# Kernel tuning notes

Hardware: AMD Instinct MI355X
Metric: run time of the kernel (lower is better)

## Reference

```python
import jax, jax.numpy as jnp
import numpy as np

GROUP_SIZE = 32


def setup_inputs() -> dict:
    key = jax.random.key(0)
    k1, k2 = jax.random.split(key)
    R, L = 4096, 16384
    G = L // GROUP_SIZE  # 512 groups
    weight = jax.random.normal(k1, (R, L), dtype=jnp.float32)
    eps_param = jnp.zeros((G,), dtype=jnp.float32)  # eps_init = 0.0
    adversarial_delta = 0.01 * jax.random.normal(k2, (G,), dtype=jnp.float32)
    return {"weight": weight, "eps_param": eps_param, "adversarial_delta": adversarial_delta}


def reference(weight, eps_param, adversarial_delta):
    L = weight.shape[-1]
    G = L // GROUP_SIZE
    # eps in [-0.5, 0.5], plus adversarial delta, clamped
    eps = 0.5 * jnp.tanh(eps_param)
    eps_eff = jnp.clip(eps + adversarial_delta, -0.5, 0.5)  # [G]

    # group along last dim; shared exponent reduces over ALL leading dims too
    wg = weight.reshape(-1, G, GROUP_SIZE)  # [R, G, gs]
    max_abs = jnp.max(jnp.abs(wg), axis=(0, 2))  # [G]
    e_base = jnp.where(max_abs > 0, jnp.floor(jnp.log2(max_abs)), 0.0)  # [G]
    # in torch, e_base comes from .item() -> constant w.r.t. autograd
    scale = jax.lax.stop_gradient(jnp.exp2(e_base))  # [G]

    s = scale[None, :, None]
    ratio = jnp.clip(jnp.abs(wg) / s, 0.0, 1.0)
    shifted = jnp.clip(ratio + eps_eff[None, :, None], 0.0, 1.0)
    mantissa_q = jnp.round(shifted * 8.0) / 8.0  # 3-bit mantissa grid
    quant = jnp.sign(wg) * s * mantissa_q

    quant_w = quant.reshape(weight.shape)
    return quant_w, jax.lax.stop_gradient(eps_eff), e_base
```

## Files before the change

### kernel.cpp

```cpp
#include <hip/hip_runtime.h>
#include <math.h>

#define NROWS 4096
#define NCOLS 16384
#define NGRP  512
#define TOTAL_ELEMS (67108864ULL)
#define TOTAL4      (16777216ULL)

typedef float nfloat4 __attribute__((ext_vector_type(4)));


__global__ void init_kernel(unsigned int* __restrict__ gmax) {
    gmax[threadIdx.x] = 0u;
}

__global__ void __launch_bounds__(256)
maxabs_kernel(const float4* __restrict__ w,
              unsigned int* __restrict__ gmax) {
    __shared__ unsigned int smax[NGRP];
    for (int i = threadIdx.x; i < NGRP; i += blockDim.x) smax[i] = 0u;
    __syncthreads();

    const size_t tid0   = (size_t)blockIdx.x * blockDim.x + threadIdx.x;
    const size_t stride = (size_t)gridDim.x * blockDim.x;
    const int g = (int)((tid0 & 4095) >> 3);

    float m0 = 0.f, m1 = 0.f;
    size_t i = tid0;
    for (; i + stride < TOTAL4; i += 2 * stride) {
        float4 a = w[i];
        float4 b = w[i + stride];
        m0 = fmaxf(m0, fmaxf(fmaxf(fabsf(a.x), fabsf(a.y)),
                             fmaxf(fabsf(a.z), fabsf(a.w))));
        m1 = fmaxf(m1, fmaxf(fmaxf(fabsf(b.x), fabsf(b.y)),
                             fmaxf(fabsf(b.z), fabsf(b.w))));
    }
    for (; i < TOTAL4; i += stride) {
        float4 a = w[i];
        m0 = fmaxf(m0, fmaxf(fmaxf(fabsf(a.x), fabsf(a.y)),
                             fmaxf(fabsf(a.z), fabsf(a.w))));
    }
    float m = fmaxf(m0, m1);

    m = fmaxf(m, __shfl_xor(m, 1, 64));
    m = fmaxf(m, __shfl_xor(m, 2, 64));
    m = fmaxf(m, __shfl_xor(m, 4, 64));
    if ((threadIdx.x & 7) == 0)
        atomicMax(&smax[g], __float_as_uint(m));

    __syncthreads();
    for (int j = threadIdx.x; j < NGRP; j += blockDim.x)
        if (smax[j]) atomicMax(&gmax[j], smax[j]);
}

__device__ __forceinline__ float quant1(float a, float s, float inv, float ee) {
    float r  = fminf(fabsf(a) * inv, 1.f);
    float sh = fminf(fmaxf(r + ee, 0.f), 1.f);
    float mq = rintf(sh * 8.f) * 0.125f;
    float q  = copysignf(s * mq, a);
    return (a == 0.f) ? 0.f : q;
}

__global__ void __launch_bounds__(256)
quant_kernel(const float4* __restrict__ w,
             const float* __restrict__ eps_param,
             const float* __restrict__ delta,
             const unsigned int* __restrict__ gmax,
             float* __restrict__ tail,
             float4* __restrict__ out) {
    const size_t tid0   = (size_t)blockIdx.x * blockDim.x + threadIdx.x;
    const size_t stride = (size_t)gridDim.x * blockDim.x;
    const int g = (int)((tid0 & 4095) >> 3);

    float ma = __uint_as_float(gmax[g]);
    float e = 0.f;
    if (ma > 0.f) {
        int ex;
        (void)frexpf(ma, &ex);
        e = (float)(ex - 1);
    }
    float eps = 0.5f * tanhf(eps_param[g]);
    float ee  = fminf(fmaxf(eps + delta[g], -0.5f), 0.5f);
    const int   ei  = (int)e;
    const float s   = __uint_as_float((unsigned)(ei + 127) << 23);
    const float inv = __uint_as_float((unsigned)(127 - ei) << 23);

    if (tid0 < 4096 && (tid0 & 7) == 0) {
        tail[g]        = ee;
        tail[NGRP + g] = e;
    }

    #pragma unroll
    for (int k = 7; k >= 0; --k) {
        size_t i = tid0 + (size_t)k * stride;
        float4 v = w[i];
        nfloat4 o;
        o.x = quant1(v.x, s, inv, ee);
        o.y = quant1(v.y, s, inv, ee);
        o.z = quant1(v.z, s, inv, ee);
        o.w = quant1(v.w, s, inv, ee);
        __builtin_nontemporal_store(o, (nfloat4*)&out[i]);
    }
}

extern "C" void kernel_launch(void* const* d_in, const int* in_sizes, int n_in,
                              void* d_out, int out_size, void* d_ws, size_t ws_size,
                              hipStream_t stream) {
    const float* weight    = (const float*)d_in[0];
    const float* eps_param = (const float*)d_in[1];
    const float* delta     = (const float*)d_in[2];
    float* out  = (float*)d_out;
    float* tail = out + TOTAL_ELEMS;
    unsigned int* gmax = (unsigned int*)d_ws;

    init_kernel<<<1, NGRP, 0, stream>>>(gmax);
    maxabs_kernel<<<2048, 256, 0, stream>>>((const float4*)weight, gmax);
    quant_kernel<<<8192, 256, 0, stream>>>((const float4*)weight, eps_param,
                                           delta, gmax, tail, (float4*)out);
}
```

Baseline: 483.7 us.

## Fuse max-abs reduction and quantization into one cooperative kernel with grid sync

Merges the max-abs pass and the quantize pass into a single cooperative kernel that reduces per-group maxima, does a grid-wide sync, then quantizes. The quantize loop walks memory in reverse so the most recently read tail of the weights may still be in cache. This removes one kernel launch boundary and may let part of the second read hit L2/MALL. In exchange it needs a cooperative launch with a fixed 1024-block grid and pays the cost of a grid barrier.

```diff
diff --git a/kernel.cpp b/kernel.cpp
--- a/kernel.cpp
+++ b/kernel.cpp
@@ -1,56 +1,23 @@
 #include <hip/hip_runtime.h>
+#include <hip/hip_cooperative_groups.h>
 #include <math.h>
+
+namespace cg = cooperative_groups;
 
 #define NROWS 4096
 #define NCOLS 16384
 #define NGRP  512
 #define TOTAL_ELEMS (67108864ULL)
 #define TOTAL4      (16777216ULL)
+#define GRID_BLOCKS 1024
+#define BLOCK 256
+#define STRIDE ((size_t)GRID_BLOCKS * BLOCK)
 
 typedef float nfloat4 __attribute__((ext_vector_type(4)));
 
 
 __global__ void init_kernel(unsigned int* __restrict__ gmax) {
     gmax[threadIdx.x] = 0u;
-}
-
-__global__ void __launch_bounds__(256)
-maxabs_kernel(const float4* __restrict__ w,
-              unsigned int* __restrict__ gmax) {
-    __shared__ unsigned int smax[NGRP];
-    for (int i = threadIdx.x; i < NGRP; i += blockDim.x) smax[i] = 0u;
-    __syncthreads();
-
-    const size_t tid0   = (size_t)blockIdx.x * blockDim.x + threadIdx.x;
-    const size_t stride = (size_t)gridDim.x * blockDim.x;
-    const int g = (int)((tid0 & 4095) >> 3);
-
-    float m0 = 0.f, m1 = 0.f;
-    size_t i = tid0;
-    for (; i + stride < TOTAL4; i += 2 * stride) {
-        float4 a = w[i];
-        float4 b = w[i + stride];
-        m0 = fmaxf(m0, fmaxf(fmaxf(fabsf(a.x), fabsf(a.y)),
-                             fmaxf(fabsf(a.z), fabsf(a.w))));
-        m1 = fmaxf(m1, fmaxf(fmaxf(fabsf(b.x), fabsf(b.y)),
-                             fmaxf(fabsf(b.z), fabsf(b.w))));
-    }
-    for (; i < TOTAL4; i += stride) {
-        float4 a = w[i];
-        m0 = fmaxf(m0, fmaxf(fmaxf(fabsf(a.x), fabsf(a.y)),
-                             fmaxf(fabsf(a.z), fabsf(a.w))));
-    }
-    float m = fmaxf(m0, m1);
-
-    m = fmaxf(m, __shfl_xor(m, 1, 64));
-    m = fmaxf(m, __shfl_xor(m, 2, 64));
-    m = fmaxf(m, __shfl_xor(m, 4, 64));
-    if ((threadIdx.x & 7) == 0)
-        atomicMax(&smax[g], __float_as_uint(m));
-
-    __syncthreads();
-    for (int j = threadIdx.x; j < NGRP; j += blockDim.x)
-        if (smax[j]) atomicMax(&gmax[j], smax[j]);
 }
 
 __device__ __forceinline__ float quant1(float a, float s, float inv, float ee) {
@@ -61,18 +28,44 @@
     return (a == 0.f) ? 0.f : q;
 }
 
-__global__ void __launch_bounds__(256)
-quant_kernel(const float4* __restrict__ w,
+__global__ void __launch_bounds__(BLOCK, 4)
+fused_kernel(const float4* __restrict__ w,
              const float* __restrict__ eps_param,
              const float* __restrict__ delta,
-             const unsigned int* __restrict__ gmax,
+             unsigned int* __restrict__ gmax,
              float* __restrict__ tail,
              float4* __restrict__ out) {
-    const size_t tid0   = (size_t)blockIdx.x * blockDim.x + threadIdx.x;
-    const size_t stride = (size_t)gridDim.x * blockDim.x;
+    __shared__ unsigned int smax[NGRP];
+    for (int i = threadIdx.x; i < NGRP; i += BLOCK) smax[i] = 0u;
+    __syncthreads();
+
+    const size_t tid0 = (size_t)blockIdx.x * BLOCK + threadIdx.x;
     const int g = (int)((tid0 & 4095) >> 3);
 
-    float ma = __uint_as_float(gmax[g]);
+    float m0 = 0.f, m1 = 0.f;
+    for (size_t i = tid0; i < TOTAL4; i += 2 * STRIDE) {
+        float4 a = w[i];
+        float4 b = w[i + STRIDE];
+        m0 = fmaxf(m0, fmaxf(fmaxf(fabsf(a.x), fabsf(a.y)),
+                             fmaxf(fabsf(a.z), fabsf(a.w))));
+        m1 = fmaxf(m1, fmaxf(fmaxf(fabsf(b.x), fabsf(b.y)),
+                             fmaxf(fabsf(b.z), fabsf(b.w))));
+    }
+    float m = fmaxf(m0, m1);
+    m = fmaxf(m, __shfl_xor(m, 1, 64));
+    m = fmaxf(m, __shfl_xor(m, 2, 64));
+    m = fmaxf(m, __shfl_xor(m, 4, 64));
+    if ((threadIdx.x & 7) == 0)
+        atomicMax(&smax[g], __float_as_uint(m));
+    __syncthreads();
+    for (int j = threadIdx.x; j < NGRP; j += BLOCK)
+        if (smax[j]) atomicMax(&gmax[j], smax[j]);
+
+    cg::this_grid().sync();
+
+    unsigned mb = __hip_atomic_load(&gmax[g], __ATOMIC_RELAXED,
+                                    __HIP_MEMORY_SCOPE_AGENT);
+    float ma = __uint_as_float(mb);
     float e = 0.f;
     if (ma > 0.f) {
         int ex;
@@ -90,31 +83,40 @@
         tail[NGRP + g] = e;
     }
 
-    #pragma unroll
-    for (int k = 7; k >= 0; --k) {
-        size_t i = tid0 + (size_t)k * stride;
-        float4 v = w[i];
-        nfloat4 o;
-        o.x = quant1(v.x, s, inv, ee);
-        o.y = quant1(v.y, s, inv, ee);
-        o.z = quant1(v.z, s, inv, ee);
-        o.w = quant1(v.w, s, inv, ee);
-        __builtin_nontemporal_store(o, (nfloat4*)&out[i]);
+    for (size_t ii = 0; ii < TOTAL4; ii += 2 * STRIDE) {
+        size_t i = (TOTAL4 - 2 * STRIDE - ii) + tid0;
+        float4 a = w[i];
+        float4 b = w[i + STRIDE];
+        nfloat4 oa, ob;
+        oa.x = quant1(a.x, s, inv, ee);
+        oa.y = quant1(a.y, s, inv, ee);
+        oa.z = quant1(a.z, s, inv, ee);
+        oa.w = quant1(a.w, s, inv, ee);
+        __builtin_nontemporal_store(oa, (nfloat4*)&out[i]);
+        ob.x = quant1(b.x, s, inv, ee);
+        ob.y = quant1(b.y, s, inv, ee);
+        ob.z = quant1(b.z, s, inv, ee);
+        ob.w = quant1(b.w, s, inv, ee);
+        __builtin_nontemporal_store(ob, (nfloat4*)&out[i + STRIDE]);
     }
 }
 
 extern "C" void kernel_launch(void* const* d_in, const int* in_sizes, int n_in,
                               void* d_out, int out_size, void* d_ws, size_t ws_size,
                               hipStream_t stream) {
-    const float* weight    = (const float*)d_in[0];
+    const float4* w4       = (const float4*)d_in[0];
     const float* eps_param = (const float*)d_in[1];
     const float* delta     = (const float*)d_in[2];
     float* out  = (float*)d_out;
     float* tail = out + TOTAL_ELEMS;
     unsigned int* gmax = (unsigned int*)d_ws;
+    float4* out4 = (float4*)out;
 
     init_kernel<<<1, NGRP, 0, stream>>>(gmax);
-    maxabs_kernel<<<2048, 256, 0, stream>>>((const float4*)weight, gmax);
-    quant_kernel<<<8192, 256, 0, stream>>>((const float4*)weight, eps_param,
-                                           delta, gmax, tail, (float4*)out);
+
+    void* args[] = { (void*)&w4, (void*)&eps_param, (void*)&delta,
+                     (void*)&gmax, (void*)&tail, (void*)&out4 };
+    hipLaunchCooperativeKernel((const void*)fused_kernel,
+                               dim3(GRID_BLOCKS), dim3(BLOCK),
+                               args, 0, stream);
 }
```

Measured after the change: 574.5 us. +18.8%, slower.
